# Kernel optimization log

Measured on AMD Instinct MI355X. Metric: run time of the kernel, lower is better.

Reference implementation:

```python
import jax, jax.numpy as jnp
import numpy as np

N_NODES = 100000
N_EDGES = 3200000
_EPS = 1e-6

# SE3 layout: [tx, ty, tz, qx, qy, qz, qw] (pypose convention)

def _normalize_se3(T):
    t, q = T[..., :3], T[..., 3:7]
    q = q / jnp.linalg.norm(q, axis=-1, keepdims=True)
    return jnp.concatenate([t, q], axis=-1)

def _qmul(q, r):
    qx, qy, qz, qw = q[..., 0], q[..., 1], q[..., 2], q[..., 3]
    rx, ry, rz, rw = r[..., 0], r[..., 1], r[..., 2], r[..., 3]
    x = qw * rx + qx * rw + qy * rz - qz * ry
    y = qw * ry - qx * rz + qy * rw + qz * rx
    z = qw * rz + qx * ry - qy * rx + qz * rw
    w = qw * rw - qx * rx - qy * ry - qz * rz
    return jnp.stack([x, y, z, w], axis=-1)

def _qrot(q, v):
    # rotate vector v by unit quaternion q: v + 2 w (u x v) + 2 u x (u x v)
    u, w = q[..., :3], q[..., 3:4]
    t = 2.0 * jnp.cross(u, v)
    return v + w * t + jnp.cross(u, t)

def _se3_inv(T):
    t, q = T[..., :3], T[..., 3:7]
    qc = q * jnp.asarray([-1.0, -1.0, -1.0, 1.0], dtype=T.dtype)
    ti = -_qrot(qc, t)
    return jnp.concatenate([ti, qc], axis=-1)

def _se3_mul(A, B):
    ta, qa = A[..., :3], A[..., 3:7]
    tb, qb = B[..., :3], B[..., 3:7]
    return jnp.concatenate([ta + _qrot(qa, tb), _qmul(qa, qb)], axis=-1)

def _so3_log(q):
    # quaternion (xyzw) -> axis-angle 3-vector
    v, w = q[..., :3], q[..., 3]
    n = jnp.linalg.norm(v, axis=-1)
    n_safe = jnp.where(n > _EPS, n, 1.0)
    scale = jnp.where(n > _EPS, 2.0 * jnp.arctan2(n, w) / n_safe, 2.0 / jnp.where(jnp.abs(w) > _EPS, w, 1.0))
    return v * scale[..., None]

def _se3_log(T):
    # SE3 -> se3 = [tau(3), phi(3)], tau = Jl(phi)^{-1} t
    t, q = T[..., :3], T[..., 3:7]
    phi = _so3_log(q)
    theta = jnp.linalg.norm(phi, axis=-1)
    small = theta < _EPS
    th = jnp.where(small, 1.0, theta)
    c = jnp.where(small, 1.0 / 12.0, 1.0 / th**2 - (1.0 + jnp.cos(th)) / (2.0 * th * jnp.sin(th)))
    pxt = jnp.cross(phi, t)
    tau = t - 0.5 * pxt + c[..., None] * jnp.cross(phi, pxt)
    return jnp.concatenate([tau, phi], axis=-1)

def setup_inputs() -> dict:
    key = jax.random.key(0)
    k1, k2, k3 = jax.random.split(key, 3)
    nodes = _normalize_se3(jax.random.normal(k1, (N_NODES, 7), dtype=jnp.float32))
    poses = _normalize_se3(jax.random.normal(k2, (N_EDGES, 7), dtype=jnp.float32))
    edges = jax.random.randint(k3, (N_EDGES, 2), 0, N_NODES, dtype=jnp.int64)
    return {"edges": edges, "poses": poses, "nodes": nodes}

def reference(edges, poses, nodes):
    node1 = nodes[edges[..., 0]]  # [E, 7]
    node2 = nodes[edges[..., 1]]  # [E, 7]
    error = _se3_mul(_se3_mul(_se3_inv(poses), node2), _se3_inv(node1))
    return _se3_log(error)  # [E, 6]
```

## Files before the change

kernel.cpp:

```cpp
#include <hip/hip_runtime.h>
#include <math.h>

#define BLOCK 256
#define EPS 1e-6f

struct F3 { float x, y, z; };
struct F4 { float x, y, z, w; };

__device__ __forceinline__ F3 cross3(F3 a, F3 b) {
    return F3{a.y * b.z - a.z * b.y,
              a.z * b.x - a.x * b.z,
              a.x * b.y - a.y * b.x};
}

__device__ __forceinline__ F3 add3(F3 a, F3 b) { return F3{a.x + b.x, a.y + b.y, a.z + b.z}; }
__device__ __forceinline__ F3 neg3(F3 a) { return F3{-a.x, -a.y, -a.z}; }

__device__ __forceinline__ F3 qrot(F4 q, F3 v) {
    F3 u{q.x, q.y, q.z};
    F3 t = cross3(u, v);
    t.x *= 2.0f; t.y *= 2.0f; t.z *= 2.0f;
    F3 c = cross3(u, t);
    return F3{v.x + q.w * t.x + c.x,
              v.y + q.w * t.y + c.y,
              v.z + q.w * t.z + c.z};
}

__device__ __forceinline__ F4 qmul(F4 q, F4 r) {
    return F4{
        q.w * r.x + q.x * r.w + q.y * r.z - q.z * r.y,
        q.w * r.y - q.x * r.z + q.y * r.w + q.z * r.x,
        q.w * r.z + q.x * r.y - q.y * r.x + q.z * r.w,
        q.w * r.w - q.x * r.x - q.y * r.y - q.z * r.z};
}

__global__ void __launch_bounds__(BLOCK) pose_graph_kernel(
    const int* __restrict__ edges,
    const float* __restrict__ poses,
    const float* __restrict__ nodes,
    float* __restrict__ out,
    int n)
{
    __shared__ float sp[BLOCK * 7];
    __shared__ float so[BLOCK * 6];

    const int tid = threadIdx.x;
    const long long base = (long long)blockIdx.x * BLOCK;
    const int limit = (int)min((long long)BLOCK, (long long)n - base);

    {
        const float* psrc = poses + base * 7;
        const int tot = limit * 7;
        #pragma unroll
        for (int k = 0; k < 7; ++k) {
            int idx = tid + k * BLOCK;
            if (idx < tot) sp[idx] = psrc[idx];
        }
    }
    __syncthreads();

    if (tid < limit) {
        const long long e = base + tid;

        const int2 ed = ((const int2*)edges)[e];

        const float* p = &sp[tid * 7];
        F3 tp{p[0], p[1], p[2]};
        F4 qp{p[3], p[4], p[5], p[6]};

        const float* n1p = nodes + (size_t)ed.x * 7;
        const float* n2p = nodes + (size_t)ed.y * 7;
        F3 t1{n1p[0], n1p[1], n1p[2]};
        F4 q1{n1p[3], n1p[4], n1p[5], n1p[6]};
        F3 t2{n2p[0], n2p[1], n2p[2]};
        F4 q2{n2p[3], n2p[4], n2p[5], n2p[6]};

        F4 qpc{-qp.x, -qp.y, -qp.z, qp.w};
        F3 tpi = neg3(qrot(qpc, tp));

        F3 tA = add3(tpi, qrot(qpc, t2));
        F4 qA = qmul(qpc, q2);

        F4 q1c{-q1.x, -q1.y, -q1.z, q1.w};
        F3 t1i = neg3(qrot(q1c, t1));

        F3 tE = add3(tA, qrot(qA, t1i));
        F4 qE = qmul(qA, q1c);

        F3 v{qE.x, qE.y, qE.z};
        float w = qE.w;
        float nn = sqrtf(v.x * v.x + v.y * v.y + v.z * v.z);
        float n_safe = (nn > EPS) ? nn : 1.0f;
        float w_safe = (fabsf(w) > EPS) ? w : 1.0f;
        float scale = (nn > EPS) ? (2.0f * atan2f(nn, w) / n_safe)
                                 : (2.0f / w_safe);
        F3 phi{v.x * scale, v.y * scale, v.z * scale};

        float theta2 = phi.x * phi.x + phi.y * phi.y + phi.z * phi.z;
        float theta = sqrtf(theta2);
        bool small = theta < EPS;
        float th = small ? 1.0f : theta;
        float s, cth;
        sincosf(th, &s, &cth);
        float c = small ? (1.0f / 12.0f)
                        : (1.0f / (th * th) - (1.0f + cth) / (2.0f * th * s));
        F3 pxt = cross3(phi, tE);
        F3 ppxt = cross3(phi, pxt);
        F3 tau{tE.x - 0.5f * pxt.x + c * ppxt.x,
               tE.y - 0.5f * pxt.y + c * ppxt.y,
               tE.z - 0.5f * pxt.z + c * ppxt.z};

        float* o = &so[tid * 6];
        o[0] = tau.x; o[1] = tau.y; o[2] = tau.z;
        o[3] = phi.x; o[4] = phi.y; o[5] = phi.z;
    }
    __syncthreads();

    {
        float* odst = out + base * 6;
        const int tot = limit * 6;
        #pragma unroll
        for (int k = 0; k < 6; ++k) {
            int idx = tid + k * BLOCK;
            if (idx < tot) odst[idx] = so[idx];
        }
    }
}

extern "C" void kernel_launch(void* const* d_in, const int* in_sizes, int n_in,
                              void* d_out, int out_size, void* d_ws, size_t ws_size,
                              hipStream_t stream) {
    const int* edges = (const int*)d_in[0];
    const float* poses = (const float*)d_in[1];
    const float* nodes = (const float*)d_in[2];
    float* out = (float*)d_out;

    const int n_edges = in_sizes[0] / 2;
    const int grid = (n_edges + BLOCK - 1) / BLOCK;

    pose_graph_kernel<<<grid, BLOCK, 0, stream>>>(edges, poses, nodes, out, n_edges);
}
```

Before: 229.4 us.

## Repack nodes to 8-float stride, process two edges per thread, use fast math

Adds a pre-pass that copies nodes into an 8-float padded workspace layout so each node gather becomes two aligned float4 loads. The main kernel handles two edges per thread with vector loads of edges, poses and outputs, dropping the shared-memory staging and block barriers. It also swaps atan2f, sqrtf, divisions and sincosf for hardware rcp/sqrt intrinsics, a polynomial atan2 and __sinf/__cosf, which trades accuracy for fewer instructions. The extra repack launch costs a small fixed amount per call.

```diff
diff --git a/kernel.cpp b/kernel.cpp
--- a/kernel.cpp
+++ b/kernel.cpp
@@ -6,13 +6,13 @@
 
 struct F3 { float x, y, z; };
 struct F4 { float x, y, z, w; };
+struct TP { F3 tau; F3 phi; };
 
 __device__ __forceinline__ F3 cross3(F3 a, F3 b) {
     return F3{a.y * b.z - a.z * b.y,
               a.z * b.x - a.x * b.z,
               a.x * b.y - a.y * b.x};
 }
-
 __device__ __forceinline__ F3 add3(F3 a, F3 b) { return F3{a.x + b.x, a.y + b.y, a.z + b.z}; }
 __device__ __forceinline__ F3 neg3(F3 a) { return F3{-a.x, -a.y, -a.z}; }
 
@@ -25,7 +25,6 @@
               v.y + q.w * t.y + c.y,
               v.z + q.w * t.z + c.z};
 }
-
 __device__ __forceinline__ F4 qmul(F4 q, F4 r) {
     return F4{
         q.w * r.x + q.x * r.w + q.y * r.z - q.z * r.y,
@@ -34,97 +33,157 @@
         q.w * r.w - q.x * r.x - q.y * r.y - q.z * r.z};
 }
 
-__global__ void __launch_bounds__(BLOCK) pose_graph_kernel(
-    const int* __restrict__ edges,
-    const float* __restrict__ poses,
-    const float* __restrict__ nodes,
-    float* __restrict__ out,
-    int n)
-{
-    __shared__ float sp[BLOCK * 7];
-    __shared__ float so[BLOCK * 6];
-
-    const int tid = threadIdx.x;
-    const long long base = (long long)blockIdx.x * BLOCK;
-    const int limit = (int)min((long long)BLOCK, (long long)n - base);
-
-    {
-        const float* psrc = poses + base * 7;
-        const int tot = limit * 7;
-        #pragma unroll
-        for (int k = 0; k < 7; ++k) {
-            int idx = tid + k * BLOCK;
-            if (idx < tot) sp[idx] = psrc[idx];
-        }
-    }
-    __syncthreads();
-
-    if (tid < limit) {
-        const long long e = base + tid;
-
-        const int2 ed = ((const int2*)edges)[e];
-
-        const float* p = &sp[tid * 7];
-        F3 tp{p[0], p[1], p[2]};
-        F4 qp{p[3], p[4], p[5], p[6]};
-
-        const float* n1p = nodes + (size_t)ed.x * 7;
-        const float* n2p = nodes + (size_t)ed.y * 7;
-        F3 t1{n1p[0], n1p[1], n1p[2]};
-        F4 q1{n1p[3], n1p[4], n1p[5], n1p[6]};
-        F3 t2{n2p[0], n2p[1], n2p[2]};
-        F4 q2{n2p[3], n2p[4], n2p[5], n2p[6]};
-
-        F4 qpc{-qp.x, -qp.y, -qp.z, qp.w};
-        F3 tpi = neg3(qrot(qpc, tp));
-
-        F3 tA = add3(tpi, qrot(qpc, t2));
-        F4 qA = qmul(qpc, q2);
-
-        F4 q1c{-q1.x, -q1.y, -q1.z, q1.w};
-        F3 t1i = neg3(qrot(q1c, t1));
-
-        F3 tE = add3(tA, qrot(qA, t1i));
-        F4 qE = qmul(qA, q1c);
-
-        F3 v{qE.x, qE.y, qE.z};
-        float w = qE.w;
-        float nn = sqrtf(v.x * v.x + v.y * v.y + v.z * v.z);
-        float n_safe = (nn > EPS) ? nn : 1.0f;
+__device__ __forceinline__ float fast_atan2(float y, float x) {
+    float ax = fabsf(x);
+    float hi = fmaxf(ax, y);
+    float lo = fminf(ax, y);
+    float r  = lo * __builtin_amdgcn_rcpf(hi);
+    float r2 = r * r;
+    float p = -0.0117212f;
+    p = fmaf(p, r2, 0.05265332f);
+    p = fmaf(p, r2, -0.11643287f);
+    p = fmaf(p, r2, 0.19354346f);
+    p = fmaf(p, r2, -0.33262347f);
+    p = fmaf(p, r2, 0.99997726f);
+    float a = r * p;
+    if (y > ax) a = 1.57079632679f - a;
+    if (x < 0.0f) a = 3.14159265359f - a;
+    return a;
+}
+
+__device__ __forceinline__ TP compute_edge(
+    F3 tp, F4 qp, F3 t1, F4 q1, F3 t2, F4 q2)
+{
+    F4 qpc{-qp.x, -qp.y, -qp.z, qp.w};
+    F3 tpi = neg3(qrot(qpc, tp));
+
+    F3 tA = add3(tpi, qrot(qpc, t2));
+    F4 qA = qmul(qpc, q2);
+
+    F4 q1c{-q1.x, -q1.y, -q1.z, q1.w};
+    F3 t1i = neg3(qrot(q1c, t1));
+
+    F3 tE = add3(tA, qrot(qA, t1i));
+    F4 qE = qmul(qA, q1c);
+
+    F3 v{qE.x, qE.y, qE.z};
+    float w = qE.w;
+    float nn = __builtin_amdgcn_sqrtf(v.x * v.x + v.y * v.y + v.z * v.z);
+    float scale;
+    if (nn > EPS) {
+        scale = 2.0f * fast_atan2(nn, w) * __builtin_amdgcn_rcpf(nn);
+    } else {
         float w_safe = (fabsf(w) > EPS) ? w : 1.0f;
-        float scale = (nn > EPS) ? (2.0f * atan2f(nn, w) / n_safe)
-                                 : (2.0f / w_safe);
-        F3 phi{v.x * scale, v.y * scale, v.z * scale};
-
-        float theta2 = phi.x * phi.x + phi.y * phi.y + phi.z * phi.z;
-        float theta = sqrtf(theta2);
-        bool small = theta < EPS;
-        float th = small ? 1.0f : theta;
-        float s, cth;
-        sincosf(th, &s, &cth);
-        float c = small ? (1.0f / 12.0f)
-                        : (1.0f / (th * th) - (1.0f + cth) / (2.0f * th * s));
-        F3 pxt = cross3(phi, tE);
-        F3 ppxt = cross3(phi, pxt);
-        F3 tau{tE.x - 0.5f * pxt.x + c * ppxt.x,
+        scale = 2.0f * __builtin_amdgcn_rcpf(w_safe);
+    }
+    F3 phi{v.x * scale, v.y * scale, v.z * scale};
+
+    float theta2 = phi.x * phi.x + phi.y * phi.y + phi.z * phi.z;
+    float theta = __builtin_amdgcn_sqrtf(theta2);
+    bool small = theta < EPS;
+    float th = small ? 1.0f : theta;
+    float s   = __sinf(th);
+    float cth = __cosf(th);
+    float c = small ? (1.0f / 12.0f)
+                    : (__builtin_amdgcn_rcpf(th * th)
+                       - (1.0f + cth) * __builtin_amdgcn_rcpf(2.0f * th * s));
+    F3 pxt  = cross3(phi, tE);
+    F3 ppxt = cross3(phi, pxt);
+    TP r;
+    r.tau = F3{tE.x - 0.5f * pxt.x + c * ppxt.x,
                tE.y - 0.5f * pxt.y + c * ppxt.y,
                tE.z - 0.5f * pxt.z + c * ppxt.z};
-
-        float* o = &so[tid * 6];
-        o[0] = tau.x; o[1] = tau.y; o[2] = tau.z;
-        o[3] = phi.x; o[4] = phi.y; o[5] = phi.z;
-    }
-    __syncthreads();
-
-    {
-        float* odst = out + base * 6;
-        const int tot = limit * 6;
-        #pragma unroll
-        for (int k = 0; k < 6; ++k) {
-            int idx = tid + k * BLOCK;
-            if (idx < tot) odst[idx] = so[idx];
-        }
-    }
+    r.phi = phi;
+    return r;
+}
+
+__global__ void __launch_bounds__(BLOCK) repack_nodes_kernel(
+    const float* __restrict__ nodes, float* __restrict__ nodes8, int total7)
+{
+    int idx = blockIdx.x * BLOCK + threadIdx.x;
+    int stride = gridDim.x * BLOCK;
+    for (; idx < total7; idx += stride) {
+        int node = idx / 7;
+        int comp = idx - node * 7;
+        nodes8[node * 8 + comp] = nodes[idx];
+    }
+}
+
+__global__ void __launch_bounds__(BLOCK, 4) pose_graph_pair_kernel(
+    const int*   __restrict__ edges,
+    const float* __restrict__ poses,
+    const float* __restrict__ nodes8,
+    float*       __restrict__ out,
+    int n)
+{
+    const long long gid = (long long)blockIdx.x * BLOCK + threadIdx.x;
+    const long long e0 = gid * 2;
+    if (e0 >= n) return;
+
+    if (e0 + 1 < n) {
+        const int4 ed = ((const int4*)edges)[gid];
+
+        const float2* pp = (const float2*)(poses + e0 * 7);
+        float2 p0 = pp[0], p1 = pp[1], p2 = pp[2], p3 = pp[3];
+        float2 p4 = pp[4], p5 = pp[5], p6 = pp[6];
+
+        const float4* nA1 = (const float4*)(nodes8 + ((size_t)ed.x << 3));
+        const float4* nA2 = (const float4*)(nodes8 + ((size_t)ed.y << 3));
+        const float4* nB1 = (const float4*)(nodes8 + ((size_t)ed.z << 3));
+        const float4* nB2 = (const float4*)(nodes8 + ((size_t)ed.w << 3));
+        float4 a1 = nA1[0], a1b = nA1[1];
+        float4 a2 = nA2[0], a2b = nA2[1];
+        float4 b1 = nB1[0], b1b = nB1[1];
+        float4 b2 = nB2[0], b2b = nB2[1];
+
+        TP r0 = compute_edge(
+            F3{p0.x, p0.y, p1.x}, F4{p1.y, p2.x, p2.y, p3.x},
+            F3{a1.x, a1.y, a1.z}, F4{a1.w, a1b.x, a1b.y, a1b.z},
+            F3{a2.x, a2.y, a2.z}, F4{a2.w, a2b.x, a2b.y, a2b.z});
+
+        TP r1 = compute_edge(
+            F3{p3.y, p4.x, p4.y}, F4{p5.x, p5.y, p6.x, p6.y},
+            F3{b1.x, b1.y, b1.z}, F4{b1.w, b1b.x, b1b.y, b1b.z},
+            F3{b2.x, b2.y, b2.z}, F4{b2.w, b2b.x, b2b.y, b2b.z});
+
+        float4* od = (float4*)(out + e0 * 6);
+        od[0] = float4{r0.tau.x, r0.tau.y, r0.tau.z, r0.phi.x};
+        od[1] = float4{r0.phi.y, r0.phi.z, r1.tau.x, r1.tau.y};
+        od[2] = float4{r1.tau.z, r1.phi.x, r1.phi.y, r1.phi.z};
+    } else {
+        const int2 ed = ((const int2*)edges)[e0];
+        const float* p = poses + e0 * 7;
+        const float4* n1p = (const float4*)(nodes8 + ((size_t)ed.x << 3));
+        const float4* n2p = (const float4*)(nodes8 + ((size_t)ed.y << 3));
+        float4 a1 = n1p[0], a1b = n1p[1];
+        float4 a2 = n2p[0], a2b = n2p[1];
+        TP r = compute_edge(
+            F3{p[0], p[1], p[2]}, F4{p[3], p[4], p[5], p[6]},
+            F3{a1.x, a1.y, a1.z}, F4{a1.w, a1b.x, a1b.y, a1b.z},
+            F3{a2.x, a2.y, a2.z}, F4{a2.w, a2b.x, a2b.y, a2b.z});
+        float* o = out + e0 * 6;
+        o[0] = r.tau.x; o[1] = r.tau.y; o[2] = r.tau.z;
+        o[3] = r.phi.x; o[4] = r.phi.y; o[5] = r.phi.z;
+    }
+}
+
+__global__ void __launch_bounds__(BLOCK) pose_graph_kernel_fallback(
+    const int* __restrict__ edges, const float* __restrict__ poses,
+    const float* __restrict__ nodes, float* __restrict__ out, int n)
+{
+    const long long e = (long long)blockIdx.x * BLOCK + threadIdx.x;
+    if (e >= n) return;
+    const int2 ed = ((const int2*)edges)[e];
+    const float* p = poses + e * 7;
+    const float* n1p = nodes + (size_t)ed.x * 7;
+    const float* n2p = nodes + (size_t)ed.y * 7;
+    TP r = compute_edge(
+        F3{p[0], p[1], p[2]}, F4{p[3], p[4], p[5], p[6]},
+        F3{n1p[0], n1p[1], n1p[2]}, F4{n1p[3], n1p[4], n1p[5], n1p[6]},
+        F3{n2p[0], n2p[1], n2p[2]}, F4{n2p[3], n2p[4], n2p[5], n2p[6]});
+    float* o = out + e * 6;
+    o[0] = r.tau.x; o[1] = r.tau.y; o[2] = r.tau.z;
+    o[3] = r.phi.x; o[4] = r.phi.y; o[5] = r.phi.z;
 }
 
 extern "C" void kernel_launch(void* const* d_in, const int* in_sizes, int n_in,
@@ -136,7 +195,19 @@
     float* out = (float*)d_out;
 
     const int n_edges = in_sizes[0] / 2;
-    const int grid = (n_edges + BLOCK - 1) / BLOCK;
-
-    pose_graph_kernel<<<grid, BLOCK, 0, stream>>>(edges, poses, nodes, out, n_edges);
-}
+    const int n_nodes = in_sizes[2] / 7;
+
+    const size_t ws_needed = (size_t)n_nodes * 8 * sizeof(float);
+    if (ws_size >= ws_needed) {
+        float* nodes8 = (float*)d_ws;
+        const int total7 = n_nodes * 7;
+        const int rgrid = (total7 + BLOCK - 1) / BLOCK;
+        repack_nodes_kernel<<<rgrid, BLOCK, 0, stream>>>(nodes, nodes8, total7);
+        const int n_pairs = (n_edges + 1) / 2;
+        const int grid = (n_pairs + BLOCK - 1) / BLOCK;
+        pose_graph_pair_kernel<<<grid, BLOCK, 0, stream>>>(edges, poses, nodes8, out, n_edges);
+    } else {
+        const int grid = (n_edges + BLOCK - 1) / BLOCK;
+        pose_graph_kernel_fallback<<<grid, BLOCK, 0, stream>>>(edges, poses, nodes, out, n_edges);
+    }
+}
```

After: 239.6 us. 4.4% more time.
